# Kernel tuning notes

Hardware: AMD Instinct MI355X
Metric: run time of the kernel (lower is better)

The kernel has to match this reference:

```python
import jax, jax.numpy as jnp
import numpy as np

N, B, D, A, E, H = 8, 32768, 128, 64, 32, 128


def setup_inputs() -> dict:
    key = jax.random.key(0)
    ks = jax.random.split(key, 22)
    g = lambda k, shape: (jax.random.normal(k, shape, dtype=jnp.float32) * 0.1)
    return {
        "states": jax.random.normal(ks[0], (N, B, D), dtype=jnp.float32),
        # per-agent DQN (2-hidden-layer MLP), stacked over agents
        "W1": g(ks[1], (N, D, H)), "b1": g(ks[2], (N, H)),
        "W2": g(ks[3], (N, H, H)), "b2": g(ks[4], (N, H)),
        "W3": g(ks[5], (N, H, A)), "b3": g(ks[6], (N, A)),
        # per-agent query MLP
        "Wq1": g(ks[7], (N, D, E)), "bq1": g(ks[8], (N, E)),
        "Wq2": g(ks[9], (N, E, E)), "bq2": g(ks[10], (N, E)),
        # per-agent key Linear
        "Wk": g(ks[11], (N, D, E)), "bk": g(ks[12], (N, E)),
        # shared scaling MLP (D->1->1)
        "Ws1": g(ks[13], (D, 1)), "bs1": g(ks[14], (1,)),
        "Ws2": g(ks[15], (1, 1)), "bs2": g(ks[16], (1,)),
        # shared constraint MLP (D->E->1)
        "Wc1": g(ks[17], (D, E)), "bc1": g(ks[18], (E,)),
        "Wc2": g(ks[19], (E, 1)), "bc2": g(ks[20], (1,)),
    }


def reference(states, W1, b1, W2, b2, W3, b3, Wq1, bq1, Wq2, bq2, Wk, bk,
              Ws1, bs1, Ws2, bs2, Wc1, bc1, Wc2, bc2):
    relu = jax.nn.relu
    # per-agent DQN -> q_values [B, N, A]
    h = relu(jnp.einsum('nbd,ndh->nbh', states, W1) + b1[:, None, :])
    h = relu(jnp.einsum('nbh,nhk->nbk', h, W2) + b2[:, None, :])
    q_values = (jnp.einsum('nbh,nha->nba', h, W3) + b3[:, None, :]).transpose(1, 0, 2)
    # per-agent keys [B, N, E]
    keys = (jnp.einsum('nbd,nde->nbe', states, Wk) + bk[:, None, :]).transpose(1, 0, 2)
    # per-agent queries [B, N, E]
    qh = relu(jnp.einsum('nbd,nde->nbe', states, Wq1) + bq1[:, None, :])
    queries = (jnp.einsum('nbe,nef->nbf', qh, Wq2) + bq2[:, None, :]).transpose(1, 0, 2)
    # attention [B, N, N]
    scores = jnp.einsum('bnd,bmd->bnm', queries, keys) / jnp.sqrt(jnp.float32(E))
    attn = jax.nn.softmax(scores, axis=-1)
    # faithful to original einsum 'bnm,bna->bna' (sums attn over m)
    weighted_qs = jnp.einsum('bnm,bna->bna', attn, q_values)
    # shared scaling MLP, sigmoid gate [B, N, 1]
    s = relu(jnp.einsum('nbd,do->nbo', states, Ws1) + bs1)
    s = jnp.einsum('nbo,op->nbp', s, Ws2) + bs2
    scaling = jax.nn.sigmoid(s.transpose(1, 0, 2))
    summed_q = jnp.mean(scaling * weighted_qs, axis=1)  # [B, A]
    # shared constraint MLP [B, N, 1] -> mean over agents [B, 1]
    c = relu(jnp.einsum('nbd,de->nbe', states, Wc1) + bc1)
    c = (jnp.einsum('nbe,eo->nbo', c, Wc2) + bc2).transpose(1, 0, 2)
    c = jnp.mean(c, axis=1)
    return summed_q + c  # [B, A]
```

## Files before the change

kernel.cpp:

```cpp
#include <hip/hip_runtime.h>
#include <hip/hip_bf16.h>

#define NAG 8
#define BATCH 32768
#define DDIM 128
#define ADIM 64
#define HDIM 128

#define NJ1 11
#define NJ2 8
#define NJ3 4
#define FB_L1 (NJ1*4)
#define FB_L2 (NJ2*4)
#define FB_L3 (NJ3*4)
#define FB_B  (FB_L2+FB_L3)
#define FB_TOT (FB_L1+FB_L2+FB_L3)
#define WAGENT (FB_TOT*512)

typedef __attribute__((ext_vector_type(8))) short bf16x8;
typedef __attribute__((ext_vector_type(4))) float f32x4;
typedef __attribute__((ext_vector_type(4))) unsigned int u32x4;

static __device__ __forceinline__ unsigned short f2bf(float f) {
  unsigned int u = __builtin_bit_cast(unsigned int, f);
  u += 0x7fffu + ((u >> 16) & 1u);
  return (unsigned short)(u >> 16);
}

static __device__ __forceinline__ unsigned int cvt_pk_bf16(float a, float b) {
  unsigned int r;
  asm("v_cvt_pk_bf16_f32 %0, %1, %2" : "=v"(r) : "v"(a), "v"(b));
  return r;
}

static __device__ __forceinline__ void gload_lds16(const void* g, void* l) {
  __builtin_amdgcn_global_load_lds(
      (const __attribute__((address_space(1))) unsigned int*)g,
      (__attribute__((address_space(3))) unsigned int*)l, 16, 0, 0);
}

__global__ void __launch_bounds__(256)
prep_weights(const float* __restrict__ W1, const float* __restrict__ W2,
             const float* __restrict__ W3, const float* __restrict__ Wc1,
             const float* __restrict__ Ws1, const float* __restrict__ b1,
             const float* __restrict__ bc1, const float* __restrict__ bs1,
             unsigned short* __restrict__ wbuf, float* __restrict__ b1e)
{
  int tid = blockIdx.x * 256 + threadIdx.x;
  if (tid < NAG * WAGENT) {
    int agent = tid / WAGENT;
    int rem   = tid % WAGENT;
    int fb = rem >> 9;
    int li = rem & 511;
    int l = li >> 3, t = li & 7;
    int lr = l & 15, lg = l >> 4;
    float v = 0.0f;
    if (fb < FB_L1) {
      int j = fb >> 2, kk = fb & 3;
      int col = j*16 + lr, k = kk*32 + lg*8 + t;
      if (col < 128)       v = W1[((size_t)agent*128 + k)*128 + col];
      else if (col < 160)  v = Wc1[k*32 + (col-128)];
      else if (col == 160) v = Ws1[k];
    } else if (fb < FB_L1 + FB_L2) {
      int f = fb - FB_L1;
      int j = f >> 2, kk = f & 3;
      int col = j*16 + lr, k = kk*32 + lg*8 + t;
      v = W2[((size_t)agent*128 + k)*128 + col];
    } else {
      int f = fb - FB_L1 - FB_L2;
      int j = f >> 2, kk = f & 3;
      int col = j*16 + lr, k = kk*32 + lg*8 + t;
      v = W3[((size_t)agent*128 + k)*64 + col];
    }
    wbuf[tid] = f2bf(v);
  }
  if (tid < NAG * 176) {
    int agent = tid / 176, col = tid % 176;
    float v = 0.0f;
    if (col < 128)       v = b1[agent*128 + col];
    else if (col < 160)  v = bc1[col - 128];
    else if (col == 160) v = bs1[0];
    b1e[tid] = v;
  }
}

__global__ void __launch_bounds__(512, 1)
qatten_main(const float* __restrict__ states,
            const float* __restrict__ b2g, const float* __restrict__ b3g,
            const float* __restrict__ ws2p, const float* __restrict__ bs2p,
            const float* __restrict__ wc2g, const float* __restrict__ bc2p,
            const unsigned short* __restrict__ wbuf,
            const float* __restrict__ b1e,
            float* __restrict__ out)
{
  __shared__ __align__(16) unsigned short bufA[FB_L1*512];
  __shared__ __align__(16) unsigned short bufB[FB_B*512];
  __shared__ __align__(16) unsigned short hlds[8 * 2048];

  const int tid  = threadIdx.x;
  const int wave = tid >> 6;
  const int lane = tid & 63;
  const int lr   = lane & 15;
  const int lg   = lane >> 4;
  const int row0 = blockIdx.x * 128 + wave * 16;

  unsigned short* hp = hlds + wave * 2048;

  const float ws2  = ws2p[0];
  const float bs2v = bs2p[0];
  const float bc2v = bc2p[0];
  const float wc2a = wc2g[lr];
  const float wc2b = wc2g[16 + lr];

  const f32x4 zero4 = {0.f, 0.f, 0.f, 0.f};

  f32x4 out_acc[NJ3];
#pragma unroll
  for (int j = 0; j < NJ3; ++j) out_acc[j] = zero4;

  {
    const char* sA = (const char*)wbuf;
    for (int c = wave; c < FB_L1; c += 8)
      gload_lds16(sA + c*1024 + lane*16, (char*)bufA + c*1024);
    const char* sB = (const char*)(wbuf + FB_L1*512);
    for (int c = wave; c < FB_B; c += 8)
      gload_lds16(sB + c*1024 + lane*16, (char*)bufB + c*1024);
  }

  f32x4 sreg[8];
  float b1n[NJ1], b2n[NJ2], b3n[NJ3];
  {
    const float* sb = states + (size_t)row0 * DDIM;
#pragma unroll
    for (int kk = 0; kk < 4; ++kk) {
      const float* p = sb + lr*DDIM + kk*32 + lg*8;
      sreg[kk*2]   = *(const f32x4*)p;
      sreg[kk*2+1] = *(const f32x4*)(p + 4);
    }
#pragma unroll
    for (int j = 0; j < NJ1; ++j) b1n[j] = b1e[j*16 + lr];
#pragma unroll
    for (int j = 0; j < NJ2; ++j) b2n[j] = b2g[j*16 + lr];
#pragma unroll
    for (int j = 0; j < NJ3; ++j) b3n[j] = b3g[j*16 + lr];
  }
  __syncthreads();

  for (int a = 0; a < NAG; ++a) {
    float b1v[NJ1], b2v[NJ2], b3v[NJ3];
#pragma unroll
    for (int j = 0; j < NJ1; ++j) b1v[j] = b1n[j];
#pragma unroll
    for (int j = 0; j < NJ2; ++j) b2v[j] = b2n[j];
#pragma unroll
    for (int j = 0; j < NJ3; ++j) b3v[j] = b3n[j];

    bf16x8 afr[4];
#pragma unroll
    for (int kk = 0; kk < 4; ++kk) {
      f32x4 v0 = sreg[kk*2], v1 = sreg[kk*2+1];
      u32x4 w;
      w[0] = cvt_pk_bf16(v0[0], v0[1]);
      w[1] = cvt_pk_bf16(v0[2], v0[3]);
      w[2] = cvt_pk_bf16(v1[0], v1[1]);
      w[3] = cvt_pk_bf16(v1[2], v1[3]);
      afr[kk] = __builtin_bit_cast(bf16x8, w);
    }

    if (a < NAG-1) {
      const float* sb = states + ((size_t)(a+1) * BATCH + row0) * DDIM;
#pragma unroll
      for (int kk = 0; kk < 4; ++kk) {
        const float* p = sb + lr*DDIM + kk*32 + lg*8;
        sreg[kk*2]   = *(const f32x4*)p;
        sreg[kk*2+1] = *(const f32x4*)(p + 4);
      }
#pragma unroll
      for (int j = 0; j < NJ1; ++j) b1n[j] = b1e[(a+1)*176 + j*16 + lr];
#pragma unroll
      for (int j = 0; j < NJ2; ++j) b2n[j] = b2g[(a+1)*HDIM + j*16 + lr];
#pragma unroll
      for (int j = 0; j < NJ3; ++j) b3n[j] = b3g[(a+1)*ADIM + j*16 + lr];
    }

    f32x4 eacc[3];
    {
      bf16x8 pf[3][4];
#pragma unroll
      for (int kk = 0; kk < 4; ++kk) {
        pf[0][kk] = *(const bf16x8*)&bufA[(0*4 + kk)*512 + lane*8];
        pf[1][kk] = *(const bf16x8*)&bufA[(1*4 + kk)*512 + lane*8];
      }
#pragma unroll
      for (int j = 0; j < 11; ++j) {
        if (j + 2 <= 10) {
#pragma unroll
          for (int kk = 0; kk < 4; ++kk)
            pf[(j+2)%3][kk] = *(const bf16x8*)&bufA[((j+2)*4 + kk)*512 + lane*8];
        }
        f32x4 acc = zero4;
#pragma unroll
        for (int kk = 0; kk < 4; ++kk)
          acc = __builtin_amdgcn_mfma_f32_16x16x32_bf16(afr[kk], pf[j%3][kk], acc, 0, 0, 0);
        if (j < 8) {
#pragma unroll
          for (int r = 0; r < 4; ++r) {
            float hv = acc[r] + b1v[j];
            hv = hv > 0.f ? hv : 0.f;
            int row = lg*4 + r;
            int bo = row*256 + (((j*16 + lr)*2) ^ ((row & 7) << 4));
            *(unsigned short*)((char*)hp + bo) = f2bf(hv);
          }
        } else {
          eacc[j-8] = acc;
        }
      }
    }

    float scl[4], crow[4];
#pragma unroll
    for (int r = 0; r < 4; ++r) {
      float c0 = eacc[0][r] + b1v[8];  c0 = c0 > 0.f ? c0 : 0.f;
      float c1 = eacc[1][r] + b1v[9];  c1 = c1 > 0.f ? c1 : 0.f;
      float cd = c0*wc2a + c1*wc2b;
      cd += __shfl_xor(cd, 1);
      cd += __shfl_xor(cd, 2);
      cd += __shfl_xor(cd, 4);
      cd += __shfl_xor(cd, 8);
      crow[r] = cd + bc2v;
      float sp = eacc[2][r] + b1v[10];
      sp = __shfl(sp, lane & 48);
      sp = sp > 0.f ? sp : 0.f;
      float s = ws2 * sp + bs2v;
      scl[r] = 1.f / (1.f + __expf(-s));
    }

#pragma unroll
    for (int kk = 0; kk < 4; ++kk) {
      int row = lr;
      int bo = row*256 + ((kk*64 + lg*16) ^ ((row & 7) << 4));
      afr[kk] = *(const bf16x8*)((char*)hp + bo);
    }

    __syncthreads();

    if (a < NAG-1) {
      const char* sA = (const char*)(wbuf + (size_t)(a+1)*WAGENT);
      for (int c = wave; c < FB_L1; c += 8)
        gload_lds16(sA + c*1024 + lane*16, (char*)bufA + c*1024);
    }

    {
      bf16x8 pf[3][4];
#pragma unroll
      for (int kk = 0; kk < 4; ++kk) {
        pf[0][kk] = *(const bf16x8*)&bufB[(0*4 + kk)*512 + lane*8];
        pf[1][kk] = *(const bf16x8*)&bufB[(1*4 + kk)*512 + lane*8];
      }
#pragma unroll
      for (int j = 0; j < 8; ++j) {
        if (j + 2 <= 7) {
#pragma unroll
          for (int kk = 0; kk < 4; ++kk)
            pf[(j+2)%3][kk] = *(const bf16x8*)&bufB[((j+2)*4 + kk)*512 + lane*8];
        }
        f32x4 acc = zero4;
#pragma unroll
        for (int kk = 0; kk < 4; ++kk)
          acc = __builtin_amdgcn_mfma_f32_16x16x32_bf16(afr[kk], pf[j%3][kk], acc, 0, 0, 0);
#pragma unroll
        for (int r = 0; r < 4; ++r) {
          float hv = acc[r] + b2v[j];
          hv = hv > 0.f ? hv : 0.f;
          int row = lg*4 + r;
          int bo = row*256 + (((j*16 + lr)*2) ^ ((row & 7) << 4));
          *(unsigned short*)((char*)hp + bo) = f2bf(hv);
        }
      }
    }

#pragma unroll
    for (int kk = 0; kk < 4; ++kk) {
      int row = lr;
      int bo = row*256 + ((kk*64 + lg*16) ^ ((row & 7) << 4));
      afr[kk] = *(const bf16x8*)((char*)hp + bo);
    }

    {
      bf16x8 pf[2][4];
#pragma unroll
      for (int kk = 0; kk < 4; ++kk)
        pf[0][kk] = *(const bf16x8*)&bufB[(FB_L2 + kk)*512 + lane*8];
#pragma unroll
      for (int j = 0; j < NJ3; ++j) {
        if (j < NJ3-1) {
#pragma unroll
          for (int kk = 0; kk < 4; ++kk)
            pf[(j+1)&1][kk] = *(const bf16x8*)&bufB[(FB_L2 + (j+1)*4 + kk)*512 + lane*8];
        }
        f32x4 acc = zero4;
#pragma unroll
        for (int kk = 0; kk < 4; ++kk)
          acc = __builtin_amdgcn_mfma_f32_16x16x32_bf16(afr[kk], pf[j&1][kk], acc, 0, 0, 0);
#pragma unroll
        for (int r = 0; r < 4; ++r)
          out_acc[j][r] += scl[r] * (acc[r] + b3v[j]) + crow[r];
      }
    }

    __syncthreads();

    if (a < NAG-1) {
      const char* sB = (const char*)(wbuf + (size_t)(a+1)*WAGENT + FB_L1*512);
      for (int c = wave; c < FB_B; c += 8)
        gload_lds16(sB + c*1024 + lane*16, (char*)bufB + c*1024);
    }
  }

#pragma unroll
  for (int j = 0; j < NJ3; ++j)
#pragma unroll
    for (int r = 0; r < 4; ++r) {
      size_t row = (size_t)row0 + lg*4 + r;
      out[row*ADIM + j*16 + lr] = out_acc[j][r] * 0.125f;
    }
}

extern "C" void kernel_launch(void* const* d_in, const int* in_sizes, int n_in,
                              void* d_out, int out_size, void* d_ws, size_t ws_size,
                              hipStream_t stream)
{
  const float* states = (const float*)d_in[0];
  const float* W1  = (const float*)d_in[1];
  const float* b1  = (const float*)d_in[2];
  const float* W2  = (const float*)d_in[3];
  const float* b2  = (const float*)d_in[4];
  const float* W3  = (const float*)d_in[5];
  const float* b3  = (const float*)d_in[6];
  const float* Ws1 = (const float*)d_in[13];
  const float* bs1 = (const float*)d_in[14];
  const float* Ws2 = (const float*)d_in[15];
  const float* bs2 = (const float*)d_in[16];
  const float* Wc1 = (const float*)d_in[17];
  const float* bc1 = (const float*)d_in[18];
  const float* Wc2 = (const float*)d_in[19];
  const float* bc2 = (const float*)d_in[20];

  unsigned short* wbuf = (unsigned short*)d_ws;
  float* b1e = (float*)((char*)d_ws + (size_t)NAG * WAGENT * 2);

  dim3 pb(256), pg((NAG * WAGENT + 255) / 256);
  prep_weights<<<pg, pb, 0, stream>>>(W1, W2, W3, Wc1, Ws1, b1, bc1, bs1, wbuf, b1e);

  dim3 mb(512), mg(BATCH / 128);
  qatten_main<<<mg, mb, 0, stream>>>(states, b2, b3, Ws2, bs2, Wc2, bc2,
                                     wbuf, b1e, (float*)d_out);
}
```

Before: 62.93 us.

## Halve block size and share one LDS weight buffer to fit two blocks per CU

Shrinks each block to 4 waves (64 rows) and merges the separate layer-1 and layer-2/3 weight buffers into one shared LDS region, so two blocks can be resident per CU. The weight loads are no longer prefetched a stage ahead. Each stage's weights are loaded right before use and followed by an extra barrier, so latency hiding now depends on the co-resident block. Bias prefetch for the next agent moves next to the layer-2 weight load. This removes the cross-stage double buffering and adds synchronization in exchange for lower LDS use and more resident waves.

Measured after the change: 61.50 us. 1.02x faster.

```diff
diff --git a/kernel.cpp b/kernel.cpp
--- a/kernel.cpp
+++ b/kernel.cpp
@@ -84,7 +84,7 @@
   }
 }
 
-__global__ void __launch_bounds__(512, 1)
+__global__ void __launch_bounds__(256, 2)
 qatten_main(const float* __restrict__ states,
             const float* __restrict__ b2g, const float* __restrict__ b3g,
             const float* __restrict__ ws2p, const float* __restrict__ bs2p,
@@ -93,16 +93,15 @@
             const float* __restrict__ b1e,
             float* __restrict__ out)
 {
-  __shared__ __align__(16) unsigned short bufA[FB_L1*512];
-  __shared__ __align__(16) unsigned short bufB[FB_B*512];
-  __shared__ __align__(16) unsigned short hlds[8 * 2048];
+  __shared__ __align__(16) unsigned short bufW[FB_B*512];
+  __shared__ __align__(16) unsigned short hlds[4 * 2048];
 
   const int tid  = threadIdx.x;
   const int wave = tid >> 6;
   const int lane = tid & 63;
   const int lr   = lane & 15;
   const int lg   = lane >> 4;
-  const int row0 = blockIdx.x * 128 + wave * 16;
+  const int row0 = blockIdx.x * 64 + wave * 16;
 
   unsigned short* hp = hlds + wave * 2048;
 
@@ -120,11 +119,8 @@
 
   {
     const char* sA = (const char*)wbuf;
-    for (int c = wave; c < FB_L1; c += 8)
-      gload_lds16(sA + c*1024 + lane*16, (char*)bufA + c*1024);
-    const char* sB = (const char*)(wbuf + FB_L1*512);
-    for (int c = wave; c < FB_B; c += 8)
-      gload_lds16(sB + c*1024 + lane*16, (char*)bufB + c*1024);
+    for (int c = wave; c < FB_L1; c += 4)
+      gload_lds16(sA + c*1024 + lane*16, (char*)bufW + c*1024);
   }
 
   f32x4 sreg[8];
@@ -175,12 +171,6 @@
         sreg[kk*2]   = *(const f32x4*)p;
         sreg[kk*2+1] = *(const f32x4*)(p + 4);
       }
-#pragma unroll
-      for (int j = 0; j < NJ1; ++j) b1n[j] = b1e[(a+1)*176 + j*16 + lr];
-#pragma unroll
-      for (int j = 0; j < NJ2; ++j) b2n[j] = b2g[(a+1)*HDIM + j*16 + lr];
-#pragma unroll
-      for (int j = 0; j < NJ3; ++j) b3n[j] = b3g[(a+1)*ADIM + j*16 + lr];
     }
 
     f32x4 eacc[3];
@@ -188,15 +178,15 @@
       bf16x8 pf[3][4];
 #pragma unroll
       for (int kk = 0; kk < 4; ++kk) {
-        pf[0][kk] = *(const bf16x8*)&bufA[(0*4 + kk)*512 + lane*8];
-        pf[1][kk] = *(const bf16x8*)&bufA[(1*4 + kk)*512 + lane*8];
+        pf[0][kk] = *(const bf16x8*)&bufW[(0*4 + kk)*512 + lane*8];
+        pf[1][kk] = *(const bf16x8*)&bufW[(1*4 + kk)*512 + lane*8];
       }
 #pragma unroll
       for (int j = 0; j < 11; ++j) {
         if (j + 2 <= 10) {
 #pragma unroll
           for (int kk = 0; kk < 4; ++kk)
-            pf[(j+2)%3][kk] = *(const bf16x8*)&bufA[((j+2)*4 + kk)*512 + lane*8];
+            pf[(j+2)%3][kk] = *(const bf16x8*)&bufW[((j+2)*4 + kk)*512 + lane*8];
         }
         f32x4 acc = zero4;
 #pragma unroll
@@ -244,25 +234,35 @@
 
     __syncthreads();
 
+    {
+      const char* sB = (const char*)(wbuf + (size_t)a*WAGENT + FB_L1*512);
+      for (int c = wave; c < FB_B; c += 4)
+        gload_lds16(sB + c*1024 + lane*16, (char*)bufW + c*1024);
+    }
     if (a < NAG-1) {
-      const char* sA = (const char*)(wbuf + (size_t)(a+1)*WAGENT);
-      for (int c = wave; c < FB_L1; c += 8)
-        gload_lds16(sA + c*1024 + lane*16, (char*)bufA + c*1024);
-    }
+#pragma unroll
+      for (int j = 0; j < NJ1; ++j) b1n[j] = b1e[(a+1)*176 + j*16 + lr];
+#pragma unroll
+      for (int j = 0; j < NJ2; ++j) b2n[j] = b2g[(a+1)*HDIM + j*16 + lr];
+#pragma unroll
+      for (int j = 0; j < NJ3; ++j) b3n[j] = b3g[(a+1)*ADIM + j*16 + lr];
+    }
+
+    __syncthreads();
 
     {
       bf16x8 pf[3][4];
 #pragma unroll
       for (int kk = 0; kk < 4; ++kk) {
-        pf[0][kk] = *(const bf16x8*)&bufB[(0*4 + kk)*512 + lane*8];
-        pf[1][kk] = *(const bf16x8*)&bufB[(1*4 + kk)*512 + lane*8];
+        pf[0][kk] = *(const bf16x8*)&bufW[(0*4 + kk)*512 + lane*8];
+        pf[1][kk] = *(const bf16x8*)&bufW[(1*4 + kk)*512 + lane*8];
       }
 #pragma unroll
       for (int j = 0; j < 8; ++j) {
         if (j + 2 <= 7) {
 #pragma unroll
           for (int kk = 0; kk < 4; ++kk)
-            pf[(j+2)%3][kk] = *(const bf16x8*)&bufB[((j+2)*4 + kk)*512 + lane*8];
+            pf[(j+2)%3][kk] = *(const bf16x8*)&bufW[((j+2)*4 + kk)*512 + lane*8];
         }
         f32x4 acc = zero4;
 #pragma unroll
@@ -290,13 +290,13 @@
       bf16x8 pf[2][4];
 #pragma unroll
       for (int kk = 0; kk < 4; ++kk)
-        pf[0][kk] = *(const bf16x8*)&bufB[(FB_L2 + kk)*512 + lane*8];
+        pf[0][kk] = *(const bf16x8*)&bufW[(FB_L2 + kk)*512 + lane*8];
 #pragma unroll
       for (int j = 0; j < NJ3; ++j) {
         if (j < NJ3-1) {
 #pragma unroll
           for (int kk = 0; kk < 4; ++kk)
-            pf[(j+1)&1][kk] = *(const bf16x8*)&bufB[(FB_L2 + (j+1)*4 + kk)*512 + lane*8];
+            pf[(j+1)&1][kk] = *(const bf16x8*)&bufW[(FB_L2 + (j+1)*4 + kk)*512 + lane*8];
         }
         f32x4 acc = zero4;
 #pragma unroll
@@ -311,10 +311,12 @@
     __syncthreads();
 
     if (a < NAG-1) {
-      const char* sB = (const char*)(wbuf + (size_t)(a+1)*WAGENT + FB_L1*512);
-      for (int c = wave; c < FB_B; c += 8)
-        gload_lds16(sB + c*1024 + lane*16, (char*)bufB + c*1024);
-    }
+      const char* sA = (const char*)(wbuf + (size_t)(a+1)*WAGENT);
+      for (int c = wave; c < FB_L1; c += 4)
+        gload_lds16(sA + c*1024 + lane*16, (char*)bufW + c*1024);
+    }
+
+    __syncthreads();
   }
 
 #pragma unroll
@@ -352,7 +354,7 @@
   dim3 pb(256), pg((NAG * WAGENT + 255) / 256);
   prep_weights<<<pg, pb, 0, stream>>>(W1, W2, W3, Wc1, Ws1, b1, bc1, bs1, wbuf, b1e);
 
-  dim3 mb(512), mg(BATCH / 128);
+  dim3 mb(256), mg(BATCH / 64);
   qatten_main<<<mg, mb, 0, stream>>>(states, b2, b3, Ws2, bs2, Wc2, bc2,
                                      wbuf, b1e, (float*)d_out);
 }
```

## Split work per agent per block, keep weights resident, combine agents with atomics

Applied to the files above, without the earlier changes.

Each block now handles a single agent over 1024 rows. That agent's full weight set is loaded into LDS once and stays there, so the per-agent weight reloads and the block barriers inside the loop go away. Results from the eight agents are combined with float atomicAdd into an output zeroed beforehand by a memset. Bf16 conversion also switches to a hardware pack instruction. The costs are 8x more atomic traffic on the output, a run-to-run nondeterministic summation order, an extra memset, and a grid of 256 blocks, which may leave compute units idle.

New measurement: 77.14 us. +22.6%, slower.

```diff
diff --git a/kernel.cpp b/kernel.cpp
--- a/kernel.cpp
+++ b/kernel.cpp
@@ -13,7 +13,6 @@
 #define FB_L1 (NJ1*4)
 #define FB_L2 (NJ2*4)
 #define FB_L3 (NJ3*4)
-#define FB_B  (FB_L2+FB_L3)
 #define FB_TOT (FB_L1+FB_L2+FB_L3)
 #define WAGENT (FB_TOT*512)
 
@@ -31,6 +30,12 @@
   unsigned int r;
   asm("v_cvt_pk_bf16_f32 %0, %1, %2" : "=v"(r) : "v"(a), "v"(b));
   return r;
+}
+
+static __device__ __forceinline__ unsigned short f2bf1(float f) {
+  unsigned int r;
+  asm("v_cvt_pk_bf16_f32 %0, %1, %2" : "=v"(r) : "v"(f), "v"(f));
+  return (unsigned short)r;
 }
 
 static __device__ __forceinline__ void gload_lds16(const void* g, void* l) {
@@ -93,8 +98,7 @@
             const float* __restrict__ b1e,
             float* __restrict__ out)
 {
-  __shared__ __align__(16) unsigned short bufA[FB_L1*512];
-  __shared__ __align__(16) unsigned short bufB[FB_B*512];
+  __shared__ __align__(16) unsigned short wlds[FB_TOT*512];
   __shared__ __align__(16) unsigned short hlds[8 * 2048];
 
   const int tid  = threadIdx.x;
@@ -102,10 +106,24 @@
   const int lane = tid & 63;
   const int lr   = lane & 15;
   const int lg   = lane >> 4;
-  const int row0 = blockIdx.x * 128 + wave * 16;
+  const int agent   = blockIdx.x >> 5;
+  const int rowbase = (blockIdx.x & 31) << 10;
 
   unsigned short* hp = hlds + wave * 2048;
 
+  {
+    const char* wag = (const char*)(wbuf + (size_t)agent * WAGENT);
+    for (int c = wave; c < FB_TOT; c += 8)
+      gload_lds16(wag + c*1024 + lane*16, (char*)wlds + c*1024);
+  }
+
+  float b1v[NJ1], b2v[NJ2], b3v[NJ3];
+#pragma unroll
+  for (int j = 0; j < NJ1; ++j) b1v[j] = b1e[agent*176 + j*16 + lr];
+#pragma unroll
+  for (int j = 0; j < NJ2; ++j) b2v[j] = b2g[agent*HDIM + j*16 + lr];
+#pragma unroll
+  for (int j = 0; j < NJ3; ++j) b3v[j] = b3g[agent*ADIM + j*16 + lr];
   const float ws2  = ws2p[0];
   const float bs2v = bs2p[0];
   const float bc2v = bc2p[0];
@@ -114,46 +132,21 @@
 
   const f32x4 zero4 = {0.f, 0.f, 0.f, 0.f};
 
-  f32x4 out_acc[NJ3];
-#pragma unroll
-  for (int j = 0; j < NJ3; ++j) out_acc[j] = zero4;
-
+  f32x4 sreg[8];
   {
-    const char* sA = (const char*)wbuf;
-    for (int c = wave; c < FB_L1; c += 8)
-      gload_lds16(sA + c*1024 + lane*16, (char*)bufA + c*1024);
-    const char* sB = (const char*)(wbuf + FB_L1*512);
-    for (int c = wave; c < FB_B; c += 8)
-      gload_lds16(sB + c*1024 + lane*16, (char*)bufB + c*1024);
-  }
-
-  f32x4 sreg[8];
-  float b1n[NJ1], b2n[NJ2], b3n[NJ3];
-  {
-    const float* sb = states + (size_t)row0 * DDIM;
+    const float* sb = states + ((size_t)agent * BATCH + rowbase + wave*16) * DDIM;
 #pragma unroll
     for (int kk = 0; kk < 4; ++kk) {
       const float* p = sb + lr*DDIM + kk*32 + lg*8;
       sreg[kk*2]   = *(const f32x4*)p;
       sreg[kk*2+1] = *(const f32x4*)(p + 4);
     }
-#pragma unroll
-    for (int j = 0; j < NJ1; ++j) b1n[j] = b1e[j*16 + lr];
-#pragma unroll
-    for (int j = 0; j < NJ2; ++j) b2n[j] = b2g[j*16 + lr];
-#pragma unroll
-    for (int j = 0; j < NJ3; ++j) b3n[j] = b3g[j*16 + lr];
-  }
+  }
+
   __syncthreads();
 
-  for (int a = 0; a < NAG; ++a) {
-    float b1v[NJ1], b2v[NJ2], b3v[NJ3];
-#pragma unroll
-    for (int j = 0; j < NJ1; ++j) b1v[j] = b1n[j];
-#pragma unroll
-    for (int j = 0; j < NJ2; ++j) b2v[j] = b2n[j];
-#pragma unroll
-    for (int j = 0; j < NJ3; ++j) b3v[j] = b3n[j];
+  for (int it = 0; it < 8; ++it) {
+    const int row0 = rowbase + it*128 + wave*16;
 
     bf16x8 afr[4];
 #pragma unroll
@@ -167,20 +160,14 @@
       afr[kk] = __builtin_bit_cast(bf16x8, w);
     }
 
-    if (a < NAG-1) {
-      const float* sb = states + ((size_t)(a+1) * BATCH + row0) * DDIM;
+    if (it < 7) {
+      const float* sb = states + ((size_t)agent * BATCH + row0 + 128) * DDIM;
 #pragma unroll
       for (int kk = 0; kk < 4; ++kk) {
         const float* p = sb + lr*DDIM + kk*32 + lg*8;
         sreg[kk*2]   = *(const f32x4*)p;
         sreg[kk*2+1] = *(const f32x4*)(p + 4);
       }
-#pragma unroll
-      for (int j = 0; j < NJ1; ++j) b1n[j] = b1e[(a+1)*176 + j*16 + lr];
-#pragma unroll
-      for (int j = 0; j < NJ2; ++j) b2n[j] = b2g[(a+1)*HDIM + j*16 + lr];
-#pragma unroll
-      for (int j = 0; j < NJ3; ++j) b3n[j] = b3g[(a+1)*ADIM + j*16 + lr];
     }
 
     f32x4 eacc[3];
@@ -188,15 +175,15 @@
       bf16x8 pf[3][4];
 #pragma unroll
       for (int kk = 0; kk < 4; ++kk) {
-        pf[0][kk] = *(const bf16x8*)&bufA[(0*4 + kk)*512 + lane*8];
-        pf[1][kk] = *(const bf16x8*)&bufA[(1*4 + kk)*512 + lane*8];
+        pf[0][kk] = *(const bf16x8*)&wlds[(0*4 + kk)*512 + lane*8];
+        pf[1][kk] = *(const bf16x8*)&wlds[(1*4 + kk)*512 + lane*8];
       }
 #pragma unroll
       for (int j = 0; j < 11; ++j) {
         if (j + 2 <= 10) {
 #pragma unroll
           for (int kk = 0; kk < 4; ++kk)
-            pf[(j+2)%3][kk] = *(const bf16x8*)&bufA[((j+2)*4 + kk)*512 + lane*8];
+            pf[(j+2)%3][kk] = *(const bf16x8*)&wlds[((j+2)*4 + kk)*512 + lane*8];
         }
         f32x4 acc = zero4;
 #pragma unroll
@@ -209,7 +196,7 @@
             hv = hv > 0.f ? hv : 0.f;
             int row = lg*4 + r;
             int bo = row*256 + (((j*16 + lr)*2) ^ ((row & 7) << 4));
-            *(unsigned short*)((char*)hp + bo) = f2bf(hv);
+            *(unsigned short*)((char*)hp + bo) = f2bf1(hv);
           }
         } else {
           eacc[j-8] = acc;
@@ -242,27 +229,19 @@
       afr[kk] = *(const bf16x8*)((char*)hp + bo);
     }
 
-    __syncthreads();
-
-    if (a < NAG-1) {
-      const char* sA = (const char*)(wbuf + (size_t)(a+1)*WAGENT);
-      for (int c = wave; c < FB_L1; c += 8)
-        gload_lds16(sA + c*1024 + lane*16, (char*)bufA + c*1024);
-    }
-
     {
       bf16x8 pf[3][4];
 #pragma unroll
       for (int kk = 0; kk < 4; ++kk) {
-        pf[0][kk] = *(const bf16x8*)&bufB[(0*4 + kk)*512 + lane*8];
-        pf[1][kk] = *(const bf16x8*)&bufB[(1*4 + kk)*512 + lane*8];
+        pf[0][kk] = *(const bf16x8*)&wlds[(FB_L1 + 0*4 + kk)*512 + lane*8];
+        pf[1][kk] = *(const bf16x8*)&wlds[(FB_L1 + 1*4 + kk)*512 + lane*8];
       }
 #pragma unroll
       for (int j = 0; j < 8; ++j) {
         if (j + 2 <= 7) {
 #pragma unroll
           for (int kk = 0; kk < 4; ++kk)
-            pf[(j+2)%3][kk] = *(const bf16x8*)&bufB[((j+2)*4 + kk)*512 + lane*8];
+            pf[(j+2)%3][kk] = *(const bf16x8*)&wlds[(FB_L1 + (j+2)*4 + kk)*512 + lane*8];
         }
         f32x4 acc = zero4;
 #pragma unroll
@@ -274,7 +253,7 @@
           hv = hv > 0.f ? hv : 0.f;
           int row = lg*4 + r;
           int bo = row*256 + (((j*16 + lr)*2) ^ ((row & 7) << 4));
-          *(unsigned short*)((char*)hp + bo) = f2bf(hv);
+          *(unsigned short*)((char*)hp + bo) = f2bf1(hv);
         }
       }
     }
@@ -290,40 +269,27 @@
       bf16x8 pf[2][4];
 #pragma unroll
       for (int kk = 0; kk < 4; ++kk)
-        pf[0][kk] = *(const bf16x8*)&bufB[(FB_L2 + kk)*512 + lane*8];
+        pf[0][kk] = *(const bf16x8*)&wlds[(FB_L1 + FB_L2 + kk)*512 + lane*8];
 #pragma unroll
       for (int j = 0; j < NJ3; ++j) {
         if (j < NJ3-1) {
 #pragma unroll
           for (int kk = 0; kk < 4; ++kk)
-            pf[(j+1)&1][kk] = *(const bf16x8*)&bufB[(FB_L2 + (j+1)*4 + kk)*512 + lane*8];
+            pf[(j+1)&1][kk] = *(const bf16x8*)&wlds[(FB_L1 + FB_L2 + (j+1)*4 + kk)*512 + lane*8];
         }
         f32x4 acc = zero4;
 #pragma unroll
         for (int kk = 0; kk < 4; ++kk)
           acc = __builtin_amdgcn_mfma_f32_16x16x32_bf16(afr[kk], pf[j&1][kk], acc, 0, 0, 0);
 #pragma unroll
-        for (int r = 0; r < 4; ++r)
-          out_acc[j][r] += scl[r] * (acc[r] + b3v[j]) + crow[r];
-      }
-    }
-
-    __syncthreads();
-
-    if (a < NAG-1) {
-      const char* sB = (const char*)(wbuf + (size_t)(a+1)*WAGENT + FB_L1*512);
-      for (int c = wave; c < FB_B; c += 8)
-        gload_lds16(sB + c*1024 + lane*16, (char*)bufB + c*1024);
-    }
-  }
-
-#pragma unroll
-  for (int j = 0; j < NJ3; ++j)
-#pragma unroll
-    for (int r = 0; r < 4; ++r) {
-      size_t row = (size_t)row0 + lg*4 + r;
-      out[row*ADIM + j*16 + lr] = out_acc[j][r] * 0.125f;
-    }
+        for (int r = 0; r < 4; ++r) {
+          float v = (scl[r] * (acc[r] + b3v[j]) + crow[r]) * 0.125f;
+          size_t row = (size_t)row0 + lg*4 + r;
+          atomicAdd(&out[row*ADIM + j*16 + lr], v);
+        }
+      }
+    }
+  }
 }
 
 extern "C" void kernel_launch(void* const* d_in, const int* in_sizes, int n_in,
@@ -349,10 +315,12 @@
   unsigned short* wbuf = (unsigned short*)d_ws;
   float* b1e = (float*)((char*)d_ws + (size_t)NAG * WAGENT * 2);
 
+  hipMemsetAsync(d_out, 0, (size_t)out_size * sizeof(float), stream);
+
   dim3 pb(256), pg((NAG * WAGENT + 255) / 256);
   prep_weights<<<pg, pb, 0, stream>>>(W1, W2, W3, Wc1, Ws1, b1, bc1, bs1, wbuf, b1e);
 
-  dim3 mb(512), mg(BATCH / 128);
+  dim3 mb(512), mg(NAG * 32);
   qatten_main<<<mg, mb, 0, stream>>>(states, b2, b3, Ws2, bs2, Wc2, bc2,
                                      wbuf, b1e, (float*)d_out);
 }
```
